# Performance work log

Hardware: AMD Instinct MI355X
Metric: run time of the kernel (lower is better)

Reference implementation:

```python
import jax, jax.numpy as jnp
import numpy as np

B, L = 2048, 8192
IN, H, OUT = 128, 512, 10
N_FRAMES = L // IN  # frame_step == frame_size -> non-overlapping unfold == reshape


def _lstm_layer(xs, W_ih, W_hh, b):
    """xs: [T, B, D_in]; returns (hs [T, B, H], h_T [B, H]).
    PyTorch gate order: i, f, g, o."""
    Bsz = xs.shape[1]
    h0 = jnp.zeros((Bsz, H), xs.dtype)
    c0 = jnp.zeros((Bsz, H), xs.dtype)

    def step(carry, x_t):
        h, c = carry
        gates = x_t @ W_ih.T + h @ W_hh.T + b  # [B, 4H]
        i, f, g, o = jnp.split(gates, 4, axis=-1)
        c = jax.nn.sigmoid(f) * c + jax.nn.sigmoid(i) * jnp.tanh(g)
        h = jax.nn.sigmoid(o) * jnp.tanh(c)
        return (h, c), h

    (hT, _), hs = jax.lax.scan(step, (h0, c0), xs)
    return hs, hT


def setup_inputs() -> dict:
    key = jax.random.key(0)
    ks = jax.random.split(key, 12)
    s_in = 1.0 / np.sqrt(H)
    return {
        "xb": jax.random.normal(ks[0], (B, L), jnp.float32),
        "W_ih0": jax.random.normal(ks[1], (4 * H, IN), jnp.float32) * s_in,
        "W_hh0": jax.random.normal(ks[2], (4 * H, H), jnp.float32) * s_in,
        "b0": jax.random.normal(ks[3], (4 * H,), jnp.float32) * s_in,
        "W_ih1": jax.random.normal(ks[4], (4 * H, H), jnp.float32) * s_in,
        "W_hh1": jax.random.normal(ks[5], (4 * H, H), jnp.float32) * s_in,
        "b1": jax.random.normal(ks[6], (4 * H,), jnp.float32) * s_in,
        "W_out": jax.random.normal(ks[7], (OUT, H), jnp.float32) * s_in,
        "b_out": jax.random.normal(ks[8], (OUT,), jnp.float32) * s_in,
    }


def reference(xb, W_ih0, W_hh0, b0, W_ih1, W_hh1, b1, W_out, b_out):
    # unfold(1, fs, fs) with step==size -> reshape; transpose to time-major
    frames = xb.reshape(B, N_FRAMES, IN).transpose(1, 0, 2)  # [T, B, IN]
    hs0, _ = _lstm_layer(frames, W_ih0, W_hh0, b0)           # [T, B, H]
    _, hT1 = _lstm_layer(hs0, W_ih1, W_hh1, b1)              # [B, H]
    return hT1 @ W_out.T + b_out                             # [B, OUT]
```

## Files before the change

kernel.cpp:

```cpp
#include <hip/hip_runtime.h>
#include <hip/hip_bf16.h>


typedef _Float16 f16x8 __attribute__((ext_vector_type(8)));
typedef float f32x4 __attribute__((ext_vector_type(4)));

#define Bsz 2048
#define Lsz 8192
#define Tsz 64
#define XSTR 258

__global__ void cvt_f32_f16(const float* __restrict__ src, _Float16* __restrict__ dst, int n4) {
    int stride = gridDim.x * blockDim.x;
    for (int i = blockIdx.x * blockDim.x + threadIdx.x; i < n4; i += stride) {
        float4 v = ((const float4*)src)[i];
        union { _Float16 h[4]; ushort4 u; } o;
        o.h[0] = (_Float16)v.x; o.h[1] = (_Float16)v.y;
        o.h[2] = (_Float16)v.z; o.h[3] = (_Float16)v.w;
        ((ushort4*)dst)[i] = o.u;
    }
}

__global__ void pack_w(const float* __restrict__ Wih, const float* __restrict__ Whh,
                       _Float16* __restrict__ dst, int K1) {
    int KT = K1 + 512;
    int n4 = 2048 * KT / 4;
    int stride = gridDim.x * blockDim.x;
    for (int i = blockIdx.x * blockDim.x + threadIdx.x; i < n4; i += stride) {
        int row = i / (KT / 4);
        int col = (i % (KT / 4)) * 4;
        const float* s = (col < K1) ? (Wih + (size_t)row * K1 + col)
                                    : (Whh + (size_t)row * 512 + (col - K1));
        float4 v = *(const float4*)s;
        union { _Float16 h[4]; ushort4 u; } o;
        o.h[0] = (_Float16)v.x; o.h[1] = (_Float16)v.y;
        o.h[2] = (_Float16)v.z; o.h[3] = (_Float16)v.w;
        ((ushort4*)dst)[i] = o.u;
    }
}

__device__ __forceinline__ float fsig(float x)  { return 1.0f / (1.0f + __expf(-x)); }
__device__ __forceinline__ float ftanh(float x) { return 1.0f - 2.0f / (__expf(2.0f * x) + 1.0f); }

__device__ __forceinline__ void gll16(const _Float16* src, char* dst) {
    __builtin_amdgcn_global_load_lds(
        (const __attribute__((address_space(1))) void*)src,
        (__attribute__((address_space(3))) void*)dst, 16, 0, 0);
}

template<int K1>
__device__ __forceinline__ void stageB(
    const _Float16* __restrict__ Wcat, int hcb, int k0, char* buf, int tid)
{
    constexpr int KT = K1 + 512;
    const int wv = tid >> 6;
#pragma unroll
    for (int qq = 0; qq < 4; ++qq) {
        const int j  = qq * 64 + (tid >> 3);
        const int cg = (((tid & 7) ^ (j & 7)) << 3);
        const int wrow = ((j >> 6) << 9) + hcb * 64 + (j & 63);
        gll16(Wcat + (size_t)wrow * KT + k0 + cg, buf + qq * 8192 + wv * 1024);
    }
}

template<int K1>
__device__ __forceinline__ void stageA(
    const _Float16* __restrict__ A1, int lda1,
    const _Float16* __restrict__ A2,
    int rowtile, int k0, char* buf, int tid)
{
    const int wv = tid >> 6;
#pragma unroll
    for (int qq = 0; qq < 2; ++qq) {
        const int row  = qq * 64 + (tid >> 3);
        const int cg   = (((tid & 7) ^ (row & 7)) << 3);
        const int brow = rowtile * 128 + row;
        char* d = buf + qq * 8192 + wv * 1024;
        if (k0 < K1) gll16(A1 + (size_t)brow * lda1 + k0 + cg, d);
        else         gll16(A2 + (size_t)brow * 512 + (k0 - K1) + cg, d);
    }
}

template<int K1>
__device__ __forceinline__ void step_v11(
    const _Float16* __restrict__ A1, int lda1,
    const _Float16* __restrict__ A2,
    const _Float16* __restrict__ Wcat,
    const float* __restrict__ bias,
    float* __restrict__ c,
    _Float16* __restrict__ h_out,
    int rowtile, int hcb, char* lds)
{
    constexpr int KT  = K1 + 512;
    constexpr int NIT = KT / 64;
    const int tid = threadIdx.x;
    const int ln  = tid & 63;
    const int wv  = tid >> 6;
    const int llo = ln & 15, lhi = ln >> 4;
    const int wr  = wv >> 2, wc = wv & 3;

    f32x4 acc[4][4] = {};

    stageA<K1>(A1, lda1, A2, rowtile, 0, lds + 65536, tid);
    stageB<K1>(Wcat, hcb, 0, lds, tid);
    stageA<K1>(A1, lda1, A2, rowtile, 64, lds + 65536 + 16384, tid);

    for (int it = 0; it < NIT; ++it) {
        if (it + 1 < NIT)
            stageB<K1>(Wcat, hcb, (it + 1) * 64, lds + ((it + 1) & 1) * 32768, tid);
        if (it + 2 < NIT)
            stageA<K1>(A1, lda1, A2, rowtile, (it + 2) * 64,
                       lds + 65536 + ((it + 2) % 3) * 16384, tid);
        if (it < NIT - 2)       asm volatile("s_waitcnt vmcnt(8)" ::: "memory");
        else if (it == NIT - 2) asm volatile("s_waitcnt vmcnt(6)" ::: "memory");
        else                    asm volatile("s_waitcnt vmcnt(0)" ::: "memory");
        __builtin_amdgcn_s_barrier();
        __builtin_amdgcn_sched_barrier(0);

        char* bb = lds + (it & 1) * 32768;
        char* ab = lds + 65536 + (it % 3) * 16384;
#pragma unroll
        for (int ks = 0; ks < 2; ++ks) {
            const int gsw = (((ks * 4 + lhi) ^ (llo & 7)) << 4);
            f16x8 a[4], b[4];
#pragma unroll
            for (int mi = 0; mi < 4; ++mi)
                a[mi] = *(const f16x8*)(ab + (wr * 64 + mi * 16 + llo) * 128 + gsw);
#pragma unroll
            for (int cf = 0; cf < 4; ++cf)
                b[cf] = *(const f16x8*)(bb + (wc * 64 + cf * 16 + llo) * 128 + gsw);
#pragma unroll
            for (int mi = 0; mi < 4; ++mi)
#pragma unroll
                for (int cf = 0; cf < 4; ++cf)
                    acc[mi][cf] = __builtin_amdgcn_mfma_f32_16x16x32_f16(
                        a[mi], b[cf], acc[mi][cf], 0, 0, 0);
        }
        __builtin_amdgcn_s_barrier();
        __builtin_amdgcn_sched_barrier(0);
    }

    float* gl = (float*)lds;
#pragma unroll
    for (int mi = 0; mi < 4; ++mi)
#pragma unroll
        for (int cf = 0; cf < 4; ++cf) {
            const int col = wc * 64 + cf * 16 + llo;
#pragma unroll
            for (int rr = 0; rr < 4; ++rr) {
                const int row = wr * 64 + mi * 16 + lhi * 4 + rr;
                gl[row * XSTR + col] = acc[mi][cf][rr];
            }
        }
    __syncthreads();

    const int lc2  = (tid & 31) << 1;
    const int ro   = tid >> 5;
    const int hcol = hcb * 64 + lc2;
    const float bi0 = bias[hcol],        bi1 = bias[hcol + 1];
    const float bf0 = bias[512 + hcol],  bf1 = bias[512 + hcol + 1];
    const float bg0 = bias[1024 + hcol], bg1 = bias[1024 + hcol + 1];
    const float bo0 = bias[1536 + hcol], bo1 = bias[1536 + hcol + 1];
#pragma unroll
    for (int i = 0; i < 8; ++i) {
        const int row = i * 16 + ro;
        const float* g0 = gl + row * XSTR + lc2;
        float iv0 = g0[0]   + bi0, iv1 = g0[1]   + bi1;
        float fv0 = g0[64]  + bf0, fv1 = g0[65]  + bf1;
        float gv0 = g0[128] + bg0, gv1 = g0[129] + bg1;
        float ov0 = g0[192] + bo0, ov1 = g0[193] + bo1;
        const size_t base = (size_t)(rowtile * 128 + row) * 512 + hcol;
        float2 cc = *(const float2*)&c[base];
        float cn0 = fsig(fv0) * cc.x + fsig(iv0) * ftanh(gv0);
        float cn1 = fsig(fv1) * cc.y + fsig(iv1) * ftanh(gv1);
        float2 cw; cw.x = cn0; cw.y = cn1;
        *(float2*)&c[base] = cw;
        float hn0 = fsig(ov0) * ftanh(cn0);
        float hn1 = fsig(ov1) * ftanh(cn1);
        union { _Float16 h2[2]; unsigned u; } hp;
        hp.h2[0] = (_Float16)hn0; hp.h2[1] = (_Float16)hn1;
        *(unsigned*)(h_out + base) = hp.u;
    }
}

__global__ __launch_bounds__(512, 1) void lstm_round(
    int t0, int t1,
    const _Float16* __restrict__ xb16,
    const _Float16* __restrict__ Wc0, const float* __restrict__ b0, float* __restrict__ c0,
    _Float16* __restrict__ h00, _Float16* __restrict__ h01,
    const _Float16* __restrict__ Wc1, const float* __restrict__ b1, float* __restrict__ c1,
    _Float16* __restrict__ h10, _Float16* __restrict__ h11)
{
    __shared__ __align__(16) char lds[132096];
    const int bid     = blockIdx.x;
    const int hcb     = bid & 7;
    const int q       = bid >> 3;
    const int layer   = q & 1;
    const int rowtile = q >> 1;

    if (layer == 0) {
        if (t0 < 0) return;
        const _Float16* hr = (t0 & 1) ? h01 : h00;
        _Float16*       hw = (t0 & 1) ? h00 : h01;
        step_v11<128>(xb16 + (size_t)t0 * 128, Lsz, hr, Wc0, b0, c0, hw, rowtile, hcb, lds);
    } else {
        if (t1 < 0) return;
        const _Float16* h0in = ((t1 + 1) & 1) ? h01 : h00;
        const _Float16* hr   = (t1 & 1) ? h11 : h10;
        _Float16*       hw   = (t1 & 1) ? h10 : h11;
        step_v11<512>(h0in, 512, hr, Wc1, b1, c1, hw, rowtile, hcb, lds);
    }
}

__global__ void proj_kernel(const _Float16* __restrict__ h1,
                            const float* __restrict__ Wout,
                            const float* __restrict__ bout,
                            float* __restrict__ out)
{
    int tid = blockIdx.x * blockDim.x + threadIdx.x;
    if (tid >= Bsz * 10) return;
    int b = tid / 10, o = tid % 10;
    float s = bout[o];
    const _Float16* hrow = h1 + (size_t)b * 512;
    const float* wrow = Wout + (size_t)o * 512;
    for (int k = 0; k < 512; ++k) s += (float)hrow[k] * wrow[k];
    out[tid] = s;
}

extern "C" void kernel_launch(void* const* d_in, const int* in_sizes, int n_in,
                              void* d_out, int out_size, void* d_ws, size_t ws_size,
                              hipStream_t stream) {
    const float* xb    = (const float*)d_in[0];
    const float* W_ih0 = (const float*)d_in[1];
    const float* W_hh0 = (const float*)d_in[2];
    const float* b0    = (const float*)d_in[3];
    const float* W_ih1 = (const float*)d_in[4];
    const float* W_hh1 = (const float*)d_in[5];
    const float* b1    = (const float*)d_in[6];
    const float* W_out = (const float*)d_in[7];
    const float* b_out = (const float*)d_in[8];
    float* out = (float*)d_out;

    char* ws = (char*)d_ws;
    size_t off = 0;
    auto alloc = [&](size_t bytes) -> void* {
        void* p = ws + off;
        off += (bytes + 255) & ~(size_t)255;
        return p;
    };
    _Float16* xb16 = (_Float16*)alloc((size_t)Bsz * Lsz * 2);
    _Float16* Wc0  = (_Float16*)alloc((size_t)2048 * 640 * 2);
    _Float16* Wc1  = (_Float16*)alloc((size_t)2048 * 1024 * 2);
    _Float16* h00  = (_Float16*)alloc((size_t)Bsz * 512 * 2);
    _Float16* h01  = (_Float16*)alloc((size_t)Bsz * 512 * 2);
    _Float16* h10  = (_Float16*)alloc((size_t)Bsz * 512 * 2);
    _Float16* h11  = (_Float16*)alloc((size_t)Bsz * 512 * 2);
    float* c0 = (float*)alloc((size_t)Bsz * 512 * 4);
    float* c1 = (float*)alloc((size_t)Bsz * 512 * 4);

    cvt_f32_f16<<<2048, 256, 0, stream>>>(xb, xb16, Bsz * Lsz / 4);
    pack_w<<<1280, 256, 0, stream>>>(W_ih0, W_hh0, Wc0, 128);
    pack_w<<<2048, 256, 0, stream>>>(W_ih1, W_hh1, Wc1, 512);

    hipMemsetAsync(h00, 0, (size_t)Bsz * 512 * 2, stream);
    hipMemsetAsync(h10, 0, (size_t)Bsz * 512 * 2, stream);
    hipMemsetAsync(c0, 0, (size_t)Bsz * 512 * 4, stream);
    hipMemsetAsync(c1, 0, (size_t)Bsz * 512 * 4, stream);

    for (int r = 0; r <= Tsz; ++r) {
        int t0 = (r < Tsz) ? r : -1;
        int t1 = r - 1;
        lstm_round<<<dim3(256), 512, 0, stream>>>(t0, t1,
            xb16, Wc0, b0, c0, h00, h01,
            Wc1, b1, c1, h10, h11);
    }

    proj_kernel<<<(Bsz * 10 + 255) / 256, 256, 0, stream>>>(h10, W_out, b_out, out);
}
```

Baseline: 1.645 ms.

## Shrink LSTM step tiles to 128x128 with gate-interleaved columns and register epilogue

Each block now computes a 128-row by 32-hidden-unit tile, covering all four gates, with 256 threads, and the grid grows to 512 blocks. Weight columns are interleaved so each wave holds i, f, g and o for the same hidden units, which lets the cell update run straight from accumulator registers instead of staging through a large LDS buffer and a sync. LDS use is halved and the A-operand prefetch goes from triple to double buffering, aiming for more blocks per CU and better occupancy across the 64-step recurrence. In exchange, each A tile is reloaded by twice as many blocks, prefetch depth is shallower, and the c and h writes become narrower scalar accesses.

```diff
diff --git a/kernel.cpp b/kernel.cpp
--- a/kernel.cpp
+++ b/kernel.cpp
@@ -8,7 +8,6 @@
 #define Bsz 2048
 #define Lsz 8192
 #define Tsz 64
-#define XSTR 258
 
 __global__ void cvt_f32_f16(const float* __restrict__ src, _Float16* __restrict__ dst, int n4) {
     int stride = gridDim.x * blockDim.x;
@@ -50,16 +49,15 @@
 
 template<int K1>
 __device__ __forceinline__ void stageB(
-    const _Float16* __restrict__ Wcat, int hcb, int k0, char* buf, int tid)
+    const _Float16* __restrict__ Wcat, int cb, int k0, char* buf, int tid)
 {
     constexpr int KT = K1 + 512;
-    const int wv = tid >> 6;
 #pragma unroll
     for (int qq = 0; qq < 4; ++qq) {
-        const int j  = qq * 64 + (tid >> 3);
+        const int j  = qq * 32 + (tid >> 3);
         const int cg = (((tid & 7) ^ (j & 7)) << 3);
-        const int wrow = ((j >> 6) << 9) + hcb * 64 + (j & 63);
-        gll16(Wcat + (size_t)wrow * KT + k0 + cg, buf + qq * 8192 + wv * 1024);
+        const int wrow = ((j >> 4) & 3) * 512 + cb * 32 + (j >> 6) * 16 + (j & 15);
+        gll16(Wcat + (size_t)wrow * KT + k0 + cg, buf + qq * 4096 + (tid >> 6) * 1024);
     }
 }
 
@@ -69,27 +67,26 @@
     const _Float16* __restrict__ A2,
     int rowtile, int k0, char* buf, int tid)
 {
-    const int wv = tid >> 6;
-#pragma unroll
-    for (int qq = 0; qq < 2; ++qq) {
-        const int row  = qq * 64 + (tid >> 3);
+#pragma unroll
+    for (int qq = 0; qq < 4; ++qq) {
+        const int row  = qq * 32 + (tid >> 3);
         const int cg   = (((tid & 7) ^ (row & 7)) << 3);
         const int brow = rowtile * 128 + row;
-        char* d = buf + qq * 8192 + wv * 1024;
+        char* d = buf + qq * 4096 + (tid >> 6) * 1024;
         if (k0 < K1) gll16(A1 + (size_t)brow * lda1 + k0 + cg, d);
         else         gll16(A2 + (size_t)brow * 512 + (k0 - K1) + cg, d);
     }
 }
 
 template<int K1>
-__device__ __forceinline__ void step_v11(
+__device__ __forceinline__ void step_v15(
     const _Float16* __restrict__ A1, int lda1,
     const _Float16* __restrict__ A2,
     const _Float16* __restrict__ Wcat,
     const float* __restrict__ bias,
     float* __restrict__ c,
     _Float16* __restrict__ h_out,
-    int rowtile, int hcb, char* lds)
+    int rowtile, int cb, char* lds)
 {
     constexpr int KT  = K1 + 512;
     constexpr int NIT = KT / 64;
@@ -97,28 +94,26 @@
     const int ln  = tid & 63;
     const int wv  = tid >> 6;
     const int llo = ln & 15, lhi = ln >> 4;
-    const int wr  = wv >> 2, wc = wv & 3;
+    const int wr  = wv >> 1, wc = wv & 1;
 
     f32x4 acc[4][4] = {};
 
-    stageA<K1>(A1, lda1, A2, rowtile, 0, lds + 65536, tid);
-    stageB<K1>(Wcat, hcb, 0, lds, tid);
-    stageA<K1>(A1, lda1, A2, rowtile, 64, lds + 65536 + 16384, tid);
+    stageA<K1>(A1, lda1, A2, rowtile, 0, lds + 32768, tid);
+    stageB<K1>(Wcat, cb, 0, lds, tid);
 
     for (int it = 0; it < NIT; ++it) {
-        if (it + 1 < NIT)
-            stageB<K1>(Wcat, hcb, (it + 1) * 64, lds + ((it + 1) & 1) * 32768, tid);
-        if (it + 2 < NIT)
-            stageA<K1>(A1, lda1, A2, rowtile, (it + 2) * 64,
-                       lds + 65536 + ((it + 2) % 3) * 16384, tid);
-        if (it < NIT - 2)       asm volatile("s_waitcnt vmcnt(8)" ::: "memory");
-        else if (it == NIT - 2) asm volatile("s_waitcnt vmcnt(6)" ::: "memory");
-        else                    asm volatile("s_waitcnt vmcnt(0)" ::: "memory");
+        if (it + 1 < NIT) {
+            stageB<K1>(Wcat, cb, (it + 1) * 64, lds + ((it + 1) & 1) * 16384, tid);
+            stageA<K1>(A1, lda1, A2, rowtile, (it + 1) * 64,
+                       lds + 32768 + ((it + 1) & 1) * 16384, tid);
+        }
+        if (it < NIT - 1) asm volatile("s_waitcnt vmcnt(8)" ::: "memory");
+        else              asm volatile("s_waitcnt vmcnt(0)" ::: "memory");
         __builtin_amdgcn_s_barrier();
         __builtin_amdgcn_sched_barrier(0);
 
-        char* bb = lds + (it & 1) * 32768;
-        char* ab = lds + 65536 + (it % 3) * 16384;
+        char* bb = lds + (it & 1) * 16384;
+        char* ab = lds + 32768 + (it & 1) * 16384;
 #pragma unroll
         for (int ks = 0; ks < 2; ++ks) {
             const int gsw = (((ks * 4 + lhi) ^ (llo & 7)) << 4);
@@ -140,50 +135,28 @@
         __builtin_amdgcn_sched_barrier(0);
     }
 
-    float* gl = (float*)lds;
+    const int hcol = cb * 32 + wc * 16 + llo;
+    float bz[4];
+#pragma unroll
+    for (int g = 0; g < 4; ++g) bz[g] = bias[g * 512 + hcol];
 #pragma unroll
     for (int mi = 0; mi < 4; ++mi)
 #pragma unroll
-        for (int cf = 0; cf < 4; ++cf) {
-            const int col = wc * 64 + cf * 16 + llo;
-#pragma unroll
-            for (int rr = 0; rr < 4; ++rr) {
-                const int row = wr * 64 + mi * 16 + lhi * 4 + rr;
-                gl[row * XSTR + col] = acc[mi][cf][rr];
-            }
+        for (int rr = 0; rr < 4; ++rr) {
+            const int row = rowtile * 128 + wr * 64 + mi * 16 + lhi * 4 + rr;
+            const size_t idx = (size_t)row * 512 + hcol;
+            float iv = acc[mi][0][rr] + bz[0];
+            float fv = acc[mi][1][rr] + bz[1];
+            float gv = acc[mi][2][rr] + bz[2];
+            float ov = acc[mi][3][rr] + bz[3];
+            float cn = fsig(fv) * c[idx] + fsig(iv) * ftanh(gv);
+            c[idx] = cn;
+            float hn = fsig(ov) * ftanh(cn);
+            h_out[idx] = (_Float16)hn;
         }
-    __syncthreads();
-
-    const int lc2  = (tid & 31) << 1;
-    const int ro   = tid >> 5;
-    const int hcol = hcb * 64 + lc2;
-    const float bi0 = bias[hcol],        bi1 = bias[hcol + 1];
-    const float bf0 = bias[512 + hcol],  bf1 = bias[512 + hcol + 1];
-    const float bg0 = bias[1024 + hcol], bg1 = bias[1024 + hcol + 1];
-    const float bo0 = bias[1536 + hcol], bo1 = bias[1536 + hcol + 1];
-#pragma unroll
-    for (int i = 0; i < 8; ++i) {
-        const int row = i * 16 + ro;
-        const float* g0 = gl + row * XSTR + lc2;
-        float iv0 = g0[0]   + bi0, iv1 = g0[1]   + bi1;
-        float fv0 = g0[64]  + bf0, fv1 = g0[65]  + bf1;
-        float gv0 = g0[128] + bg0, gv1 = g0[129] + bg1;
-        float ov0 = g0[192] + bo0, ov1 = g0[193] + bo1;
-        const size_t base = (size_t)(rowtile * 128 + row) * 512 + hcol;
-        float2 cc = *(const float2*)&c[base];
-        float cn0 = fsig(fv0) * cc.x + fsig(iv0) * ftanh(gv0);
-        float cn1 = fsig(fv1) * cc.y + fsig(iv1) * ftanh(gv1);
-        float2 cw; cw.x = cn0; cw.y = cn1;
-        *(float2*)&c[base] = cw;
-        float hn0 = fsig(ov0) * ftanh(cn0);
-        float hn1 = fsig(ov1) * ftanh(cn1);
-        union { _Float16 h2[2]; unsigned u; } hp;
-        hp.h2[0] = (_Float16)hn0; hp.h2[1] = (_Float16)hn1;
-        *(unsigned*)(h_out + base) = hp.u;
-    }
-}
-
-__global__ __launch_bounds__(512, 1) void lstm_round(
+}
+
+__global__ __launch_bounds__(256) void lstm_round(
     int t0, int t1,
     const _Float16* __restrict__ xb16,
     const _Float16* __restrict__ Wc0, const float* __restrict__ b0, float* __restrict__ c0,
@@ -191,24 +164,25 @@
     const _Float16* __restrict__ Wc1, const float* __restrict__ b1, float* __restrict__ c1,
     _Float16* __restrict__ h10, _Float16* __restrict__ h11)
 {
-    __shared__ __align__(16) char lds[132096];
+    __shared__ __align__(16) char lds[65536];
     const int bid     = blockIdx.x;
-    const int hcb     = bid & 7;
-    const int q       = bid >> 3;
-    const int layer   = q & 1;
-    const int rowtile = q >> 1;
+    const int x       = bid & 7;
+    const int rest    = bid >> 3;
+    const int layer   = rest & 1;
+    const int cb      = x * 2 + ((rest >> 1) & 1);
+    const int rowtile = rest >> 2;
 
     if (layer == 0) {
         if (t0 < 0) return;
         const _Float16* hr = (t0 & 1) ? h01 : h00;
         _Float16*       hw = (t0 & 1) ? h00 : h01;
-        step_v11<128>(xb16 + (size_t)t0 * 128, Lsz, hr, Wc0, b0, c0, hw, rowtile, hcb, lds);
+        step_v15<128>(xb16 + (size_t)t0 * 128, Lsz, hr, Wc0, b0, c0, hw, rowtile, cb, lds);
     } else {
         if (t1 < 0) return;
         const _Float16* h0in = ((t1 + 1) & 1) ? h01 : h00;
         const _Float16* hr   = (t1 & 1) ? h11 : h10;
         _Float16*       hw   = (t1 & 1) ? h10 : h11;
-        step_v11<512>(h0in, 512, hr, Wc1, b1, c1, hw, rowtile, hcb, lds);
+        step_v15<512>(h0in, 512, hr, Wc1, b1, c1, hw, rowtile, cb, lds);
     }
 }
 
@@ -270,7 +244,7 @@
     for (int r = 0; r <= Tsz; ++r) {
         int t0 = (r < Tsz) ? r : -1;
         int t1 = r - 1;
-        lstm_round<<<dim3(256), 512, 0, stream>>>(t0, t1,
+        lstm_round<<<dim3(512), 256, 0, stream>>>(t0, t1,
             xb16, Wc0, b0, c0, h00, h01,
             Wc1, b1, c1, h10, h11);
     }
```

Measured after the change: 1.535 ms. 1.07x faster.
